# Optimization experiments

Hardware: AMD Instinct MI355X
Metric: run time of the kernel (lower is better)

The kernel has to match this reference:

```python
import jax, jax.numpy as jnp
import numpy as np

N = 25000      # nodes
E = 300000     # edges
IN = 32        # in_dim
EDF = 16       # edge_feat_dim
HID = 256      # hidden_dim (per-head dim, concat=False)
HEADS = 4
ACT = 16       # num_actions
G = 64         # graphs in batch
KW = 1024      # wire-mask query nodes


def setup_inputs() -> dict:
    key = jax.random.key(0)
    ks = jax.random.split(key, 20)
    def rn(k, shape, s=0.1):
        return jax.random.normal(k, shape, jnp.float32) * s
    return {
        "x": jax.random.normal(ks[0], (N, IN), jnp.float32),
        "edge_attr": jax.random.normal(ks[1], (E, EDF), jnp.float32),
        "wire_mask": jax.random.randint(ks[2], (KW,), 0, N, jnp.int32),
        "edge_index": jax.random.randint(ks[3], (2, E), 0, N, jnp.int32),
        "batch": jnp.sort(jax.random.randint(ks[4], (N,), 0, G, jnp.int32)),
        "enc_w1": rn(ks[5], (EDF, 32)),
        "enc_b1": jnp.zeros((32,), jnp.float32),
        "enc_w2": rn(ks[6], (32, IN * IN), 0.05),
        "enc_b2": jnp.zeros((IN * IN,), jnp.float32),
        "root_w": rn(ks[7], (IN, IN)),
        "nn_bias": jnp.zeros((IN,), jnp.float32),
        "gat1_w": rn(ks[8], (IN, HEADS * HID)),
        "gat1_asrc": rn(ks[9], (HEADS, HID)),
        "gat1_adst": rn(ks[10], (HEADS, HID)),
        "gat1_b": jnp.zeros((HID,), jnp.float32),
        "gat2_w": rn(ks[11], (HID, HEADS * HID)),
        "gat2_asrc": rn(ks[12], (HEADS, HID)),
        "gat2_adst": rn(ks[13], (HEADS, HID)),
        "gat2_b": jnp.zeros((HID,), jnp.float32),
        "wire_w": rn(ks[14], (HID, 1)),
        "wire_b": jnp.zeros((1,), jnp.float32),
        "act_w": rn(ks[15], (HID, ACT)),
        "act_b": jnp.zeros((ACT,), jnp.float32),
    }


def _gat(x, src, dst, W, a_src, a_dst, b):
    # PyG GATConv, concat=False (mean over heads), eval mode (no dropout),
    # self-loops already included in (src, dst).
    H, D = a_src.shape
    h = (x @ W).reshape(-1, H, D)                      # [N, H, D]
    es = (h * a_src[None]).sum(-1)                     # [N, H]
    ed = (h * a_dst[None]).sum(-1)                     # [N, H]
    e = jax.nn.leaky_relu(es[src] + ed[dst], negative_slope=0.2)  # [E2, H]
    m = jax.ops.segment_max(e, dst, num_segments=N)    # segment softmax (stable)
    w = jnp.exp(e - m[dst])
    den = jax.ops.segment_sum(w, dst, num_segments=N)
    alpha = w / (den[dst] + 1e-16)
    out = jax.ops.segment_sum(h[src] * alpha[..., None], dst, num_segments=N)
    return out.mean(axis=1) + b                        # [N, D]


def reference(x, edge_attr, wire_mask, edge_index, batch,
              enc_w1, enc_b1, enc_w2, enc_b2, root_w, nn_bias,
              gat1_w, gat1_asrc, gat1_adst, gat1_b,
              gat2_w, gat2_asrc, gat2_adst, gat2_b,
              wire_w, wire_b, act_w, act_b):
    src, dst = edge_index[0], edge_index[1]
    # NNConv (aggr='mean'): per-edge weight matrix from edge MLP
    We = (jax.nn.relu(edge_attr @ enc_w1 + enc_b1) @ enc_w2 + enc_b2)
    We = We.reshape(E, IN, IN)                         # [E, in, out]
    msg = jnp.einsum('ei,eio->eo', x[src], We)         # [E, out]
    s = jax.ops.segment_sum(msg, dst, num_segments=N)
    cnt = jax.ops.segment_sum(jnp.ones((E,), x.dtype), dst, num_segments=N)
    agg = s / jnp.maximum(cnt, 1.0)[:, None]
    h0 = jax.nn.relu(agg + x @ root_w + nn_bias)
    # GATConv default add_self_loops=True
    sl = jnp.arange(N, dtype=src.dtype)
    src2 = jnp.concatenate([src, sl])
    dst2 = jnp.concatenate([dst, sl])
    h1 = jax.nn.relu(_gat(h0, src2, dst2, gat1_w, gat1_asrc, gat1_adst, gat1_b))
    h2 = jax.nn.relu(_gat(h1, src2, dst2, gat2_w, gat2_asrc, gat2_adst, gat2_b))
    p_wire = (h2[wire_mask] @ wire_w + wire_b).squeeze(-1)   # [KW]
    pooled_s = jax.ops.segment_sum(h2, batch, num_segments=G)
    gc = jax.ops.segment_sum(jnp.ones((N,), h2.dtype), batch, num_segments=G)
    pooled = pooled_s / jnp.maximum(gc, 1.0)[:, None]        # global_mean_pool
    p_action = pooled @ act_w + act_b                        # [G, ACT]
    return (p_wire, p_action)
```

## Files before the change

### kernel.cpp

```cpp
#include <hip/hip_runtime.h>
#include <hip/hip_fp16.h>

#define N_NODES 25000
#define M_PAD   25024
#define N_TILES 1564
#define N_EDGES 300000
#define IN_DIM  32
#define EDFD    16
#define HIDD    256
#define HEADS   4
#define NACT    16
#define NGRAPH  64
#define KWIRE   1024
#define POOL_NB 64

typedef _Float16 half8v __attribute__((ext_vector_type(8)));
typedef __attribute__((ext_vector_type(4))) float f32x4;

__device__ __forceinline__ float leaky(float v) { return v > 0.f ? v : 0.2f * v; }

__global__ __launch_bounds__(256) void k_deg2(const int* __restrict__ ei,
                                              int* __restrict__ deg,
                                              int* __restrict__ deg2) {
    int e = blockIdx.x * 256 + threadIdx.x;
    if (e >= N_EDGES) return;
    atomicAdd(&deg[ei[N_EDGES + e]], 1);
    atomicAdd(&deg2[ei[e]], 1);
}

__global__ __launch_bounds__(256) void k_scan2(const int* __restrict__ degA, int* __restrict__ rpA,
                                               const int* __restrict__ degB, int* __restrict__ rpB) {
    const int* deg = blockIdx.x ? degB : degA;
    int* rowptr    = blockIdx.x ? rpB : rpA;
    __shared__ int part[256];
    int t = threadIdx.x;
    const int CH = 98;
    int base = t * CH;
    int s = 0;
    for (int i = 0; i < CH; ++i) {
        int idx = base + i;
        if (idx < N_NODES) s += deg[idx];
    }
    part[t] = s;
    __syncthreads();
    if (t == 0) {
        int run = 0;
        for (int i = 0; i < 256; ++i) { int v = part[i]; part[i] = run; run += v; }
    }
    __syncthreads();
    int run = part[t];
    for (int i = 0; i < CH; ++i) {
        int idx = base + i;
        if (idx < N_NODES) { rowptr[idx] = run; run += deg[idx]; }
    }
    if (N_NODES >= base && N_NODES < base + CH) rowptr[N_NODES] = run;
}

__global__ __launch_bounds__(256) void k_scatter2(const int* __restrict__ ei,
                                                  const float* __restrict__ ea,
                                                  const int* __restrict__ rowptr,
                                                  const int* __restrict__ rowptr2,
                                                  int* __restrict__ cursor,
                                                  int* __restrict__ cursor2,
                                                  int* __restrict__ csrc,
                                                  int* __restrict__ cdst,
                                                  int* __restrict__ posMap,
                                                  __half* __restrict__ eaP) {
    int e = blockIdx.x * 256 + threadIdx.x;
    if (e >= N_EDGES) return;
    int src = ei[e], dst = ei[N_EDGES + e];
    int p1 = atomicAdd(&cursor[dst], 1);
    int r1 = rowptr[dst] + p1;
    csrc[r1] = src;
    int p2 = atomicAdd(&cursor2[src], 1);
    int r2 = rowptr2[src] + p2;
    cdst[r2] = dst;
    posMap[r2] = r1;
    const float4* src4 = (const float4*)(ea + (size_t)e * EDFD);
    __half2* dp = (__half2*)(eaP + (size_t)r2 * EDFD);
    #pragma unroll
    for (int q = 0; q < EDFD / 4; ++q) {
        float4 v = src4[q];
        dp[q * 2]     = __float22half2_rn(make_float2(v.x, v.y));
        dp[q * 2 + 1] = __float22half2_rn(make_float2(v.z, v.w));
    }
}

__global__ __launch_bounds__(256) void k_prep(const float* __restrict__ w2,
                                              const float* __restrict__ W1,
                                              const float* __restrict__ W2,
                                              const float* __restrict__ a1s,
                                              const float* __restrict__ a1d,
                                              const float* __restrict__ a2s,
                                              const float* __restrict__ a2d,
                                              const float* __restrict__ x,
                                              const float* __restrict__ b2,
                                              const float* __restrict__ w1,
                                              __half* __restrict__ wtt,
                                              __half* __restrict__ wb1,
                                              __half* __restrict__ wb2,
                                              float* __restrict__ wa1,
                                              float* __restrict__ wd1,
                                              float* __restrict__ wa2,
                                              float* __restrict__ wd2,
                                              __half* __restrict__ xf,
                                              float* __restrict__ xb,
                                              __half* __restrict__ w1t) {
    int bid = blockIdx.x, t = threadIdx.x;
    if (bid < 128) {
        int idx = bid * 256 + t;
        int co = idx >> 5, i = idx & 31;
        wtt[idx] = __float2half(w2[(co >> 5) * 1024 + i * 32 + (co & 31)]);
    } else if (bid < 256) {
        int idx = (bid - 128) * 256 + t;
        int d = idx >> 7, k = idx & 127;
        int h = k >> 5, i = k & 31;
        wb1[idx] = __float2half(0.25f * W1[i * 1024 + h * 256 + d]);
    } else if (bid < 1280) {
        int idx = (bid - 256) * 256 + t;
        int d = idx >> 10, k = idx & 1023;
        int h = k >> 8, i = k & 255;
        wb2[idx] = __float2half(0.25f * W2[i * 1024 + h * 256 + d]);
    } else if (bid < 4405) {
        int idx = (bid - 1280) * 256 + t;
        if (idx >= N_NODES * 32) return;
        int n = idx >> 5, o = idx & 31;
        xf[idx] = __float2half(x[idx]);
        float s = 0.f;
        for (int i = 0; i < 32; ++i) s += x[n * 32 + i] * b2[i * 32 + o];
        xb[idx] = s;
    } else if (bid == 4405) {
        if (t >= 128) return;
        int h = t >> 5, i = t & 31;
        float s = 0.f, sd = 0.f;
        for (int d = 0; d < 256; ++d) {
            float w = W1[i * 1024 + h * 256 + d];
            s  += w * a1s[h * 256 + d];
            sd += w * a1d[h * 256 + d];
        }
        wa1[t] = s; wd1[t] = sd;
    } else if (bid < 4410) {
        int idx = (bid - 4406) * 256 + t;
        if (idx >= 1024) return;
        int h = idx >> 8, i = idx & 255;
        float s = 0.f, sd = 0.f;
        for (int d = 0; d < 256; ++d) {
            float w = W2[i * 1024 + h * 256 + d];
            s  += w * a2s[h * 256 + d];
            sd += w * a2d[h * 256 + d];
        }
        wa2[idx] = s; wd2[idx] = sd;
    } else {
        int idx = (bid - 4410) * 256 + t;
        if (idx >= 32 * EDFD) return;
        int j = idx >> 4, k = idx & 15;
        w1t[idx] = __float2half(w1[k * 32 + j]);
    }
}

__global__ __launch_bounds__(256) void k_msg3(const int* __restrict__ rowptr2,
                                              const int* __restrict__ posMap,
                                              const __half* __restrict__ eaP,
                                              const __half* __restrict__ w1t,
                                              const float* __restrict__ b1,
                                              const __half* __restrict__ T,
                                              const float* __restrict__ xb,
                                              __half* __restrict__ msgE) {
    int wv = threadIdx.x >> 6, lane = threadIdx.x & 63;
    int src = blockIdx.x * 4 + wv;
    if (src >= N_NODES) return;
    int r0 = rowptr2[src], r1 = rowptr2[src + 1];
    if (r0 == r1) return;
    int lr = lane & 15, lk = (lane >> 4) * 8;

    half8v bf0, bf1;
    const __half* Tp = T + (size_t)src * 1024;
    #pragma unroll
    for (int q = 0; q < 8; ++q) {
        bf0[q] = (_Float16)__half2float(Tp[(lk + q) * 32 + lr]);
        bf1[q] = (_Float16)__half2float(Tp[(lk + q) * 32 + 16 + lr]);
    }

    __half2 w1r[8][EDFD / 2];
    #pragma unroll
    for (int q = 0; q < 8; ++q) {
        const __half2* wp = (const __half2*)(w1t + (lk + q) * EDFD);
        #pragma unroll
        for (int k2 = 0; k2 < EDFD / 2; ++k2) w1r[q][k2] = wp[k2];
    }
    float b1r[8];
    #pragma unroll
    for (int q = 0; q < 8; ++q) b1r[q] = b1[lk + q];

    float xb0 = xb[src * 32 + lr], xb1 = xb[src * 32 + 16 + lr];
    int rbase = (lane >> 4) * 4;

    for (int t0 = r0; t0 < r1; t0 += 16) {
        int e = t0 + lr;
        bool ok = (e < r1);
        half8v afr;
        if (ok) {
            const __half2* ep = (const __half2*)(eaP + (size_t)e * EDFD);
            __half2 ea2[EDFD / 2];
            #pragma unroll
            for (int k2 = 0; k2 < EDFD / 2; ++k2) ea2[k2] = ep[k2];
            #pragma unroll
            for (int q = 0; q < 8; ++q) {
                float s = b1r[q];
                #pragma unroll
                for (int k2 = 0; k2 < EDFD / 2; ++k2) {
                    float2 v = __half22float2(ea2[k2]);
                    float2 w = __half22float2(w1r[q][k2]);
                    s += v.x * w.x + v.y * w.y;
                }
                afr[q] = (_Float16)fmaxf(s, 0.f);
            }
        } else {
            #pragma unroll
            for (int q = 0; q < 8; ++q) afr[q] = (_Float16)0.f;
        }
        f32x4 c0 = {0.f, 0.f, 0.f, 0.f}, c1 = {0.f, 0.f, 0.f, 0.f};
        c0 = __builtin_amdgcn_mfma_f32_16x16x32_f16(afr, bf0, c0, 0, 0, 0);
        c1 = __builtin_amdgcn_mfma_f32_16x16x32_f16(afr, bf1, c1, 0, 0, 0);
        #pragma unroll
        for (int r = 0; r < 4; ++r) {
            int er = t0 + rbase + r;
            if (er < r1) {
                int pm = posMap[er];
                msgE[(size_t)pm * 32 + lr]      = __float2half(c0[r] + xb0);
                msgE[(size_t)pm * 32 + 16 + lr] = __float2half(c1[r] + xb1);
            }
        }
    }
}

__global__ __launch_bounds__(256) void k_h0e(const float* __restrict__ x,
                                             const float* __restrict__ root_w,
                                             const float* __restrict__ nn_bias,
                                             const __half* __restrict__ msgE,
                                             const int* __restrict__ rowptr,
                                             const float* __restrict__ wa,
                                             const float* __restrict__ wd,
                                             __half* __restrict__ h0f,
                                             float* __restrict__ es,
                                             float* __restrict__ ed) {
    int t = threadIdx.x;
    int ng = t >> 5, o = t & 31;
    int n = blockIdx.x * 8 + ng;
    if (n >= N_NODES) return;
    float s = nn_bias[o];
    for (int k = 0; k < IN_DIM; ++k) s += x[n * IN_DIM + k] * root_w[k * 32 + o];
    int r0 = rowptr[n], r1 = rowptr[n + 1];
    float aggv = 0.f;
    for (int r = r0; r < r1; ++r)
        aggv += __half2float(msgE[(size_t)r * 32 + o]);
    float c = fmaxf((float)(r1 - r0), 1.f);
    s += aggv / c;
    float v = fmaxf(s, 0.f);
    h0f[n * IN_DIM + o] = __float2half(v);
    #pragma unroll
    for (int h = 0; h < 4; ++h) {
        float ss = v * wa[h * 32 + o];
        float dd = v * wd[h * 32 + o];
        #pragma unroll
        for (int off = 16; off; off >>= 1) {
            ss += __shfl_down(ss, off, 32);
            dd += __shfl_down(dd, off, 32);
        }
        if (o == 0) { es[n * 4 + h] = ss; ed[n * 4 + h] = dd; }
    }
}

__global__ __launch_bounds__(256, 2) void k_gemT(const __half* __restrict__ A,
                                                 const __half* __restrict__ Wt,
                                                 __half* __restrict__ C) {
    __shared__ __half cst[4][16 * 36];
    int t = threadIdx.x, wid = t >> 6, lane = t & 63;
    int lr = lane & 15, lk = (lane >> 4) * 8;

    int bid = blockIdx.x;
    int xcd = bid & 7, j = bid >> 3;
    int sx = j & 31;
    int y = ((j >> 5) << 3) | xcd;
    int n0 = sx * 32;

    half8v bfr[2];
    #pragma unroll
    for (int c = 0; c < 2; ++c)
        bfr[c] = *(const half8v*)(Wt + (size_t)(n0 + c * 16 + lr) * 32 + lk);

    int tb = (y * 4 + wid) * 4;
    for (int pp = 0; pp < 4; pp += 2) {
        int tA = tb + pp;
        if (tA >= N_TILES) break;
        int mA = tA * 16, mB = mA + 16;
        half8v aA = *(const half8v*)(A + (size_t)(mA + lr) * 32 + lk);
        half8v aB = *(const half8v*)(A + (size_t)(mB + lr) * 32 + lk);
        f32x4 acc[2][2];
        #pragma unroll
        for (int i = 0; i < 2; ++i)
            #pragma unroll
            for (int c = 0; c < 2; ++c)
                acc[i][c] = (f32x4){0.f, 0.f, 0.f, 0.f};
        acc[0][0] = __builtin_amdgcn_mfma_f32_16x16x32_f16(aA, bfr[0], acc[0][0], 0, 0, 0);
        acc[0][1] = __builtin_amdgcn_mfma_f32_16x16x32_f16(aA, bfr[1], acc[0][1], 0, 0, 0);
        acc[1][0] = __builtin_amdgcn_mfma_f32_16x16x32_f16(aB, bfr[0], acc[1][0], 0, 0, 0);
        acc[1][1] = __builtin_amdgcn_mfma_f32_16x16x32_f16(aB, bfr[1], acc[1][1], 0, 0, 0);

        int rbase = (lane >> 4) * 4;
        #pragma unroll
        for (int ti = 0; ti < 2; ++ti) {
            #pragma unroll
            for (int c = 0; c < 2; ++c)
                #pragma unroll
                for (int r = 0; r < 4; ++r)
                    cst[wid][(rbase + r) * 36 + c * 16 + lr] = __float2half(acc[ti][c][r]);
            int m0 = ti ? mB : mA;
            #pragma unroll
            for (int p = 0; p < 2; ++p) {
                int row = p * 8 + (lane >> 3), hb = lane & 7;
                float2 v = *(const float2*)((const char*)&cst[wid][0] + row * 72 + hb * 8);
                *(float2*)((char*)C + ((size_t)(m0 + row) * 1024 + n0) * 2 + hb * 8) = v;
            }
        }
    }
}

template <int K, typename OT, bool FUSE_ED>
__global__ __launch_bounds__(256, 3) void k_gemmo(const __half* __restrict__ A,
                                                  const __half* __restrict__ Wt,
                                                  const float* __restrict__ bias,
                                                  OT* __restrict__ C,
                                                  const float* __restrict__ wa,
                                                  const float* __restrict__ wd,
                                                  float* __restrict__ es,
                                                  float* __restrict__ ed) {
    constexpr int CK  = 128;
    constexpr int KC  = K / CK;
    constexpr int KSC = CK / 32;
    constexpr int CB  = CK * 2;
    __shared__ __half bs[2][64 * CK];
    __shared__ float cst[4][16 * 36];
    int t = threadIdx.x, wid = t >> 6, lane = t & 63;
    int lr = lane & 15, lk = (lane >> 4) * 8;

    int bid = blockIdx.x;
    int xcd = bid & 7, rest = bid >> 3;
    int strip = rest & 3, yhi = rest >> 2;
    int y = yhi * 8 + xcd;
    if (y >= 196) return;
    int n0 = strip * 64;
    float bv[4];
    #pragma unroll
    for (int c = 0; c < 4; ++c) bv[c] = bias[n0 + c * 16 + lr];
    int tb = y * 8 + wid * 2;
    int tA0 = tb     < N_TILES ? tb     : N_TILES - 1;
    int tA1 = tb + 1 < N_TILES ? tb + 1 : N_TILES - 1;
    const int swz = (lr & 7) << 4;

    f32x4 acc[2][4];
    #pragma unroll
    for (int i = 0; i < 2; ++i)
        #pragma unroll
        for (int c = 0; c < 4; ++c)
            acc[i][c] = (f32x4){0.f, 0.f, 0.f, 0.f};

    for (int i = t * 16; i < 64 * CB; i += 256 * 16) {
        int col = i / CB, offb = i % CB;
        const char* src = (const char*)Wt + ((size_t)(n0 + col) * K) * 2 + offb;
        *(float4*)((char*)bs[0] + (i ^ ((col & 7) << 4))) = *(const float4*)src;
    }
    __syncthreads();

    const __half* pA0 = A + (size_t)(tA0 * 16 + lr) * K + lk;
    const __half* pA1 = A + (size_t)(tA1 * 16 + lr) * K + lk;

    for (int kc = 0; kc < KC; ++kc) {
        int cur = kc & 1;
        if (kc + 1 < KC) {
            for (int i = t * 16; i < 64 * CB; i += 256 * 16) {
                int col = i / CB, offb = i % CB;
                const char* src = (const char*)Wt + (((size_t)(n0 + col) * K + (kc + 1) * CK) * 2 + offb);
                *(float4*)((char*)bs[cur ^ 1] + (i ^ ((col & 7) << 4))) = *(const float4*)src;
            }
        }
        half8v aH0[KSC], aH1[KSC];
        #pragma unroll
        for (int ks = 0; ks < KSC; ++ks) {
            aH0[ks] = *(const half8v*)(pA0 + kc * CK + ks * 32);
            aH1[ks] = *(const half8v*)(pA1 + kc * CK + ks * 32);
        }
        #pragma unroll
        for (int ks = 0; ks < KSC; ++ks) {
            #pragma unroll
            for (int c = 0; c < 4; ++c) {
                half8v b = *(const half8v*)((const char*)bs[cur] +
                            (((c * 16 + lr) * CB + lk * 2 + ks * 64) ^ swz));
                acc[0][c] = __builtin_amdgcn_mfma_f32_16x16x32_f16(aH0[ks], b, acc[0][c], 0, 0, 0);
                acc[1][c] = __builtin_amdgcn_mfma_f32_16x16x32_f16(aH1[ks], b, acc[1][c], 0, 0, 0);
            }
        }
        if (kc + 1 < KC) __syncthreads();
    }

    int rbase = (lane >> 4) * 4;
    #pragma unroll
    for (int ti = 0; ti < 2; ++ti) {
        if (tb + ti >= N_TILES) break;
        int m0 = (tb + ti) * 16;
        int row = lane >> 2, cg = lane & 3;
        #pragma unroll
        for (int half = 0; half < 2; ++half) {
            #pragma unroll
            for (int c = 0; c < 2; ++c)
                #pragma unroll
                for (int r = 0; r < 4; ++r)
                    cst[wid][(rbase + r) * 36 + c * 16 + lr] =
                        fmaxf(acc[ti][half * 2 + c][r] + bv[half * 2 + c], 0.f);
            int colb = n0 + half * 32;
            const float* sp = &cst[wid][row * 36 + cg * 8];
            if constexpr (sizeof(OT) == 2) {
                __half2 o0 = __float22half2_rn(make_float2(sp[0], sp[1]));
                __half2 o1 = __float22half2_rn(make_float2(sp[2], sp[3]));
                __half2 o2 = __float22half2_rn(make_float2(sp[4], sp[5]));
                __half2 o3 = __float22half2_rn(make_float2(sp[6], sp[7]));
                float4 v = make_float4(__uint_as_float(*(unsigned*)&o0), __uint_as_float(*(unsigned*)&o1),
                                       __uint_as_float(*(unsigned*)&o2), __uint_as_float(*(unsigned*)&o3));
                *(float4*)((__half*)C + (size_t)(m0 + row) * 256 + colb + cg * 8) = v;
            } else {
                float4 v0 = make_float4(sp[0], sp[1], sp[2], sp[3]);
                float4 v1 = make_float4(sp[4], sp[5], sp[6], sp[7]);
                float* cp = (float*)C + (size_t)(m0 + row) * 256 + colb + cg * 8;
                *(float4*)cp = v0;
                *(float4*)(cp + 4) = v1;
            }
            if constexpr (FUSE_ED) {
                int rowg = m0 + row;
                #pragma unroll
                for (int h = 0; h < 4; ++h) {
                    float pes = 0.f, ped = 0.f;
                    #pragma unroll
                    for (int d = 0; d < 8; ++d) {
                        float vv = sp[d];
                        pes += vv * wa[h * 256 + colb + cg * 8 + d];
                        ped += vv * wd[h * 256 + colb + cg * 8 + d];
                    }
                    pes += __shfl_down(pes, 1, 4); pes += __shfl_down(pes, 2, 4);
                    ped += __shfl_down(ped, 1, 4); ped += __shfl_down(ped, 2, 4);
                    if (cg == 0 && rowg < N_NODES) {
                        atomicAdd(&es[rowg * 4 + h], pes);
                        atomicAdd(&ed[rowg * 4 + h], ped);
                    }
                }
            }
        }
    }
}

__global__ __launch_bounds__(256) void k_agg1(const int* __restrict__ rowptr,
                                              const int* __restrict__ csrc,
                                              const float* __restrict__ es,
                                              const float* __restrict__ ed,
                                              const __half* __restrict__ h0f,
                                              __half* __restrict__ agg0) {
    int dst = blockIdx.x * 4 + (threadIdx.x >> 6);
    if (dst >= N_NODES) return;
    int lane = threadIdx.x & 63;
    int h = lane >> 4, i2 = lane & 15;
    float edv = ed[dst * 4 + h];
    float vself = leaky(es[dst * 4 + h] + edv);
    float dn = 1.f;
    int r0 = rowptr[dst], r1 = rowptr[dst + 1];

    __half2 hv = *(const __half2*)(h0f + (size_t)dst * 32 + i2 * 2);
    float2 f = __half22float2(hv);
    float ax = f.x, ay = f.y;
    for (int r = r0; r < r1; ++r) {
        int src = csrc[r];
        float w = __expf(leaky(es[src * 4 + h] + edv) - vself);
        dn += w;
        __half2 sv = *(const __half2*)(h0f + (size_t)src * 32 + i2 * 2);
        float2 g = __half22float2(sv);
        ax += w * g.x; ay += w * g.y;
    }
    float inv = 1.f / (dn + 1e-16f);
    *(__half2*)(agg0 + (size_t)dst * 128 + h * 32 + i2 * 2) =
        __float22half2_rn(make_float2(ax * inv, ay * inv));
}

__global__ __launch_bounds__(256) void k_agg2(const int* __restrict__ rowptr,
                                              const int* __restrict__ csrc,
                                              const float* __restrict__ es,
                                              const float* __restrict__ ed,
                                              const __half* __restrict__ h1f,
                                              __half* __restrict__ agg1) {
    int dst = blockIdx.x * 4 + (threadIdx.x >> 6);
    if (dst >= N_NODES) return;
    int lane = threadIdx.x & 63;
    float vs[4], edv[4], dn[4];
    float acc[4][4];
    {
        float2 q = *(const float2*)(h1f + (size_t)dst * 256 + lane * 4);
        const __half2* hq = (const __half2*)&q;
        float2 f0 = __half22float2(hq[0]), f1 = __half22float2(hq[1]);
        #pragma unroll
        for (int h = 0; h < 4; ++h) {
            edv[h] = ed[dst * 4 + h];
            vs[h] = leaky(es[dst * 4 + h] + edv[h]);
            dn[h] = 1.f;
            acc[h][0] = f0.x; acc[h][1] = f0.y;
            acc[h][2] = f1.x; acc[h][3] = f1.y;
        }
    }
    int r0 = rowptr[dst], r1 = rowptr[dst + 1];
    for (int r = r0; r < r1; ++r) {
        int src = csrc[r];
        float4 esv = *(const float4*)(es + (size_t)src * 4);
        float w0 = __expf(leaky(esv.x + edv[0]) - vs[0]);
        float w1 = __expf(leaky(esv.y + edv[1]) - vs[1]);
        float w2 = __expf(leaky(esv.z + edv[2]) - vs[2]);
        float w3 = __expf(leaky(esv.w + edv[3]) - vs[3]);
        dn[0] += w0; dn[1] += w1; dn[2] += w2; dn[3] += w3;
        float2 q = *(const float2*)(h1f + (size_t)src * 256 + lane * 4);
        const __half2* hq = (const __half2*)&q;
        float2 f0 = __half22float2(hq[0]), f1 = __half22float2(hq[1]);
        acc[0][0] += w0 * f0.x; acc[0][1] += w0 * f0.y; acc[0][2] += w0 * f1.x; acc[0][3] += w0 * f1.y;
        acc[1][0] += w1 * f0.x; acc[1][1] += w1 * f0.y; acc[1][2] += w1 * f1.x; acc[1][3] += w1 * f1.y;
        acc[2][0] += w2 * f0.x; acc[2][1] += w2 * f0.y; acc[2][2] += w2 * f1.x; acc[2][3] += w2 * f1.y;
        acc[3][0] += w3 * f0.x; acc[3][1] += w3 * f0.y; acc[3][2] += w3 * f1.x; acc[3][3] += w3 * f1.y;
    }
    #pragma unroll
    for (int h = 0; h < 4; ++h) {
        float inv = 1.f / (dn[h] + 1e-16f);
        __half2 o0 = __float22half2_rn(make_float2(acc[h][0] * inv, acc[h][1] * inv));
        __half2 o1 = __float22half2_rn(make_float2(acc[h][2] * inv, acc[h][3] * inv));
        __half2* op = (__half2*)(agg1 + (size_t)dst * 1024 + h * 256 + lane * 4);
        op[0] = o0; op[1] = o1;
    }
}

__global__ __launch_bounds__(256) void k_wirepool(const int* __restrict__ wm,
                                                  const float* __restrict__ h2,
                                                  const float* __restrict__ ww,
                                                  const float* __restrict__ wb,
                                                  const int* __restrict__ batch,
                                                  float* __restrict__ out,
                                                  float* __restrict__ pooled,
                                                  float* __restrict__ gcnt) {
    int bid = blockIdx.x;
    if (bid < KWIRE / 4) {
        int k = bid * 4 + (threadIdx.x >> 6);
        int lane = threadIdx.x & 63;
        int n = wm[k];
        float s = 0.f;
        for (int d = lane; d < 256; d += 64) s += h2[(size_t)n * 256 + d] * ww[d];
        #pragma unroll
        for (int off = 32; off; off >>= 1) s += __shfl_down(s, off);
        if (lane == 0) out[k] = s + wb[0];
        return;
    }
    int n0 = (bid - KWIRE / 4) * POOL_NB;
    int n1 = n0 + POOL_NB; if (n1 > N_NODES) n1 = N_NODES;
    int d = threadIdx.x;
    int cur = batch[n0];
    float acc = 0.f, cnt = 0.f;
    for (int n = n0; n < n1; ++n) {
        int g = batch[n];
        if (g != cur) {
            atomicAdd(&pooled[cur * 256 + d], acc);
            if (d == 0) atomicAdd(&gcnt[cur], cnt);
            acc = 0.f; cnt = 0.f; cur = g;
        }
        acc += h2[(size_t)n * 256 + d];
        cnt += 1.f;
    }
    atomicAdd(&pooled[cur * 256 + d], acc);
    if (d == 0) atomicAdd(&gcnt[cur], cnt);
}

__global__ __launch_bounds__(256) void k_act(const float* __restrict__ pooled,
                                             const float* __restrict__ gcnt,
                                             const float* __restrict__ aw,
                                             const float* __restrict__ ab,
                                             float* __restrict__ out) {
    int u = blockIdx.x * 4 + (threadIdx.x >> 6);
    int lane = threadIdx.x & 63;
    if (u >= NGRAPH * NACT) return;
    int g = u >> 4, a = u & 15;
    float c = fmaxf(gcnt[g], 1.f);
    float s = 0.f;
    for (int d = lane; d < 256; d += 64) s += pooled[g * 256 + d] * aw[d * 16 + a];
    #pragma unroll
    for (int off = 32; off; off >>= 1) s += __shfl_down(s, off);
    if (lane == 0) out[KWIRE + u] = s / c + ab[a];
}

extern "C" void kernel_launch(void* const* d_in, const int* in_sizes, int n_in,
                              void* d_out, int out_size, void* d_ws, size_t ws_size,
                              hipStream_t stream) {
    const float* x        = (const float*)d_in[0];
    const float* edge_attr= (const float*)d_in[1];
    const int*   wire_mask= (const int*)d_in[2];
    const int*   edge_idx = (const int*)d_in[3];
    const int*   batch    = (const int*)d_in[4];
    const float* enc_w1   = (const float*)d_in[5];
    const float* enc_b1   = (const float*)d_in[6];
    const float* enc_w2   = (const float*)d_in[7];
    const float* enc_b2   = (const float*)d_in[8];
    const float* root_w   = (const float*)d_in[9];
    const float* nn_bias  = (const float*)d_in[10];
    const float* gat1_w   = (const float*)d_in[11];
    const float* gat1_asrc= (const float*)d_in[12];
    const float* gat1_adst= (const float*)d_in[13];
    const float* gat1_b   = (const float*)d_in[14];
    const float* gat2_w   = (const float*)d_in[15];
    const float* gat2_asrc= (const float*)d_in[16];
    const float* gat2_adst= (const float*)d_in[17];
    const float* gat2_b   = (const float*)d_in[18];
    const float* wire_w   = (const float*)d_in[19];
    const float* wire_b   = (const float*)d_in[20];
    const float* act_w    = (const float*)d_in[21];
    const float* act_b    = (const float*)d_in[22];
    float* out = (float*)d_out;

    float* ws = (float*)d_ws;
    size_t off = 0;
    __half* T16   = (__half*)(ws + off); off += (size_t)M_PAD * 1024 / 2;
    __half* agg1f = (__half*)(ws + off); off += (size_t)M_PAD * 1024 / 2;
    __half* agg0f = (__half*)(ws + off); off += (size_t)M_PAD * 128 / 2;
    __half* h0f   = (__half*)(ws + off); off += (size_t)M_PAD * 32 / 2;
    __half* h1f   = (__half*)(ws + off); off += (size_t)M_PAD * 256 / 2;
    __half* xf    = (__half*)(ws + off); off += (size_t)M_PAD * 32 / 2;
    __half* eaP   = (__half*)(ws + off); off += (size_t)N_EDGES * EDFD / 2;
    __half* msgE  = (__half*)(ws + off); off += (size_t)N_EDGES * 32 / 2;
    float* xb     = ws + off; off += 800000;
    float* esb    = ws + off; off += 100000;
    float* edb    = ws + off; off += 100000;
    float* h2     = ws + off; off += (size_t)M_PAD * 256;
    float* pooled = ws + off; off += NGRAPH * 256;
    float* gcnt   = ws + off; off += NGRAPH;
    int* deg      = (int*)(ws + off); off += 25600;
    int* deg2     = (int*)(ws + off); off += 25600;
    int* cursor   = (int*)(ws + off); off += 25600;
    int* cursor2  = (int*)(ws + off); off += 25600;
    int* rowptr   = (int*)(ws + off); off += 25600;
    int* rowptr2  = (int*)(ws + off); off += 25600;
    int* csrc     = (int*)(ws + off); off += N_EDGES;
    int* cdst     = (int*)(ws + off); off += N_EDGES;
    int* posMap   = (int*)(ws + off); off += N_EDGES;
    __half* wtt   = (__half*)(ws + off); off += 16384;
    __half* wb1t  = (__half*)(ws + off); off += 16384;
    __half* wb2t  = (__half*)(ws + off); off += 131072;
    __half* w1t   = (__half*)(ws + off); off += 256;
    float* wa1    = ws + off; off += 128;
    float* wd1    = ws + off; off += 128;
    float* wa2    = ws + off; off += 1024;
    float* wd2    = ws + off; off += 1024;
    float* esb2   = ws + off; off += 100000;
    float* edb2   = ws + off; off += 100000;

    const int GBT = 3328;
    const int GBO = 800;

    hipMemsetAsync(deg, 0, 4 * 25600 * sizeof(int), stream);
    hipMemsetAsync(esb2, 0, 2 * 100000 * sizeof(float), stream);
    k_deg2<<<(N_EDGES + 255) / 256, 256, 0, stream>>>(edge_idx, deg, deg2);
    k_scan2<<<2, 256, 0, stream>>>(deg, rowptr, deg2, rowptr2);
    k_scatter2<<<(N_EDGES + 255) / 256, 256, 0, stream>>>(edge_idx, edge_attr, rowptr, rowptr2,
                                                          cursor, cursor2, csrc, cdst, posMap, eaP);

    k_prep<<<4412, 256, 0, stream>>>(enc_w2, gat1_w, gat2_w, gat1_asrc, gat1_adst,
                                     gat2_asrc, gat2_adst, x, enc_b2, enc_w1,
                                     wtt, wb1t, wb2t, wa1, wd1, wa2, wd2, xf, xb, w1t);

    k_gemT<<<GBT, 256, 0, stream>>>(xf, wtt, T16);
    k_msg3<<<(N_NODES + 3) / 4, 256, 0, stream>>>(rowptr2, posMap, eaP,
                                                  w1t, enc_b1, T16, xb, msgE);
    k_h0e<<<(N_NODES + 7) / 8, 256, 0, stream>>>(x, root_w, nn_bias, msgE, rowptr,
                                                 wa1, wd1, h0f, esb, edb);

    k_agg1<<<(N_NODES + 3) / 4, 256, 0, stream>>>(rowptr, csrc, esb, edb, h0f, agg0f);
    k_gemmo<128, __half, true><<<GBO, 256, 0, stream>>>(agg0f, wb1t, gat1_b, h1f,
                                                        wa2, wd2, esb2, edb2);

    k_agg2<<<(N_NODES + 3) / 4, 256, 0, stream>>>(rowptr, csrc, esb2, edb2, h1f, agg1f);
    k_gemmo<1024, float, false><<<GBO, 256, 0, stream>>>(agg1f, wb2t, gat2_b, h2,
                                                         nullptr, nullptr, nullptr, nullptr);

    hipMemsetAsync(pooled, 0, (NGRAPH * 256 + NGRAPH) * sizeof(float), stream);
    k_wirepool<<<KWIRE / 4 + (N_NODES + POOL_NB - 1) / POOL_NB, 256, 0, stream>>>(
        wire_mask, h2, wire_w, wire_b, batch, out, pooled, gcnt);
    k_act<<<NGRAPH * NACT / 4, 256, 0, stream>>>(pooled, gcnt, act_w, act_b, out);
}
```

Before: 418.2 us.

## Fuse per-source T GEMM into message kernel, removing T16 buffer

The separate k_gemT kernel, which wrote a 25k×1024 half-precision T matrix to global memory, is removed. Each wave in k_msg3 now computes its source node's 1024-entry T row on the fly with 64 MFMA calls (only row 0 of each output tile is used) and stages it in shared memory before building the B fragments. This drops a ~51MB write and its later read, at the cost of redundant MFMA work (15 of 16 rows wasted) and repeated reads of the weight matrix per wave.

Result: slower. 536.1 us (+28.2%).

```diff
diff --git a/kernel.cpp b/kernel.cpp
--- a/kernel.cpp
+++ b/kernel.cpp
@@ -163,9 +163,11 @@
                                               const __half* __restrict__ eaP,
                                               const __half* __restrict__ w1t,
                                               const float* __restrict__ b1,
-                                              const __half* __restrict__ T,
+                                              const __half* __restrict__ xf,
+                                              const __half* __restrict__ wtt,
                                               const float* __restrict__ xb,
                                               __half* __restrict__ msgE) {
+    __shared__ __half Tl[4][1024];
     int wv = threadIdx.x >> 6, lane = threadIdx.x & 63;
     int src = blockIdx.x * 4 + wv;
     if (src >= N_NODES) return;
@@ -173,12 +175,20 @@
     if (r0 == r1) return;
     int lr = lane & 15, lk = (lane >> 4) * 8;
 
+    half8v af16 = *(const half8v*)(xf + (size_t)src * 32 + lk);
+    #pragma unroll 8
+    for (int c = 0; c < 64; ++c) {
+        half8v bw = *(const half8v*)(wtt + (size_t)(c * 16 + lr) * 32 + lk);
+        f32x4 d = {0.f, 0.f, 0.f, 0.f};
+        d = __builtin_amdgcn_mfma_f32_16x16x32_f16(af16, bw, d, 0, 0, 0);
+        if (lane < 16) Tl[wv][c * 16 + lane] = __float2half(d[0]);
+    }
+
     half8v bf0, bf1;
-    const __half* Tp = T + (size_t)src * 1024;
     #pragma unroll
     for (int q = 0; q < 8; ++q) {
-        bf0[q] = (_Float16)__half2float(Tp[(lk + q) * 32 + lr]);
-        bf1[q] = (_Float16)__half2float(Tp[(lk + q) * 32 + 16 + lr]);
+        bf0[q] = (_Float16)__half2float(Tl[wv][(lk + q) * 32 + lr]);
+        bf1[q] = (_Float16)__half2float(Tl[wv][(lk + q) * 32 + 16 + lr]);
     }
 
     __half2 w1r[8][EDFD / 2];
@@ -268,61 +278,6 @@
             dd += __shfl_down(dd, off, 32);
         }
         if (o == 0) { es[n * 4 + h] = ss; ed[n * 4 + h] = dd; }
-    }
-}
-
-__global__ __launch_bounds__(256, 2) void k_gemT(const __half* __restrict__ A,
-                                                 const __half* __restrict__ Wt,
-                                                 __half* __restrict__ C) {
-    __shared__ __half cst[4][16 * 36];
-    int t = threadIdx.x, wid = t >> 6, lane = t & 63;
-    int lr = lane & 15, lk = (lane >> 4) * 8;
-
-    int bid = blockIdx.x;
-    int xcd = bid & 7, j = bid >> 3;
-    int sx = j & 31;
-    int y = ((j >> 5) << 3) | xcd;
-    int n0 = sx * 32;
-
-    half8v bfr[2];
-    #pragma unroll
-    for (int c = 0; c < 2; ++c)
-        bfr[c] = *(const half8v*)(Wt + (size_t)(n0 + c * 16 + lr) * 32 + lk);
-
-    int tb = (y * 4 + wid) * 4;
-    for (int pp = 0; pp < 4; pp += 2) {
-        int tA = tb + pp;
-        if (tA >= N_TILES) break;
-        int mA = tA * 16, mB = mA + 16;
-        half8v aA = *(const half8v*)(A + (size_t)(mA + lr) * 32 + lk);
-        half8v aB = *(const half8v*)(A + (size_t)(mB + lr) * 32 + lk);
-        f32x4 acc[2][2];
-        #pragma unroll
-        for (int i = 0; i < 2; ++i)
-            #pragma unroll
-            for (int c = 0; c < 2; ++c)
-                acc[i][c] = (f32x4){0.f, 0.f, 0.f, 0.f};
-        acc[0][0] = __builtin_amdgcn_mfma_f32_16x16x32_f16(aA, bfr[0], acc[0][0], 0, 0, 0);
-        acc[0][1] = __builtin_amdgcn_mfma_f32_16x16x32_f16(aA, bfr[1], acc[0][1], 0, 0, 0);
-        acc[1][0] = __builtin_amdgcn_mfma_f32_16x16x32_f16(aB, bfr[0], acc[1][0], 0, 0, 0);
-        acc[1][1] = __builtin_amdgcn_mfma_f32_16x16x32_f16(aB, bfr[1], acc[1][1], 0, 0, 0);
-
-        int rbase = (lane >> 4) * 4;
-        #pragma unroll
-        for (int ti = 0; ti < 2; ++ti) {
-            #pragma unroll
-            for (int c = 0; c < 2; ++c)
-                #pragma unroll
-                for (int r = 0; r < 4; ++r)
-                    cst[wid][(rbase + r) * 36 + c * 16 + lr] = __float2half(acc[ti][c][r]);
-            int m0 = ti ? mB : mA;
-            #pragma unroll
-            for (int p = 0; p < 2; ++p) {
-                int row = p * 8 + (lane >> 3), hb = lane & 7;
-                float2 v = *(const float2*)((const char*)&cst[wid][0] + row * 72 + hb * 8);
-                *(float2*)((char*)C + ((size_t)(m0 + row) * 1024 + n0) * 2 + hb * 8) = v;
-            }
-        }
     }
 }
 
@@ -625,7 +580,6 @@
 
     float* ws = (float*)d_ws;
     size_t off = 0;
-    __half* T16   = (__half*)(ws + off); off += (size_t)M_PAD * 1024 / 2;
     __half* agg1f = (__half*)(ws + off); off += (size_t)M_PAD * 1024 / 2;
     __half* agg0f = (__half*)(ws + off); off += (size_t)M_PAD * 128 / 2;
     __half* h0f   = (__half*)(ws + off); off += (size_t)M_PAD * 32 / 2;
@@ -659,7 +613,6 @@
     float* esb2   = ws + off; off += 100000;
     float* edb2   = ws + off; off += 100000;
 
-    const int GBT = 3328;
     const int GBO = 800;
 
     hipMemsetAsync(deg, 0, 4 * 25600 * sizeof(int), stream);
@@ -673,9 +626,8 @@
                                      gat2_asrc, gat2_adst, x, enc_b2, enc_w1,
                                      wtt, wb1t, wb2t, wa1, wd1, wa2, wd2, xf, xb, w1t);
 
-    k_gemT<<<GBT, 256, 0, stream>>>(xf, wtt, T16);
     k_msg3<<<(N_NODES + 3) / 4, 256, 0, stream>>>(rowptr2, posMap, eaP,
-                                                  w1t, enc_b1, T16, xb, msgE);
+                                                  w1t, enc_b1, xf, wtt, xb, msgE);
     k_h0e<<<(N_NODES + 7) / 8, 256, 0, stream>>>(x, root_w, nn_bias, msgE, rowptr,
                                                  wa1, wd1, h0f, esb, edb);
 
```
